# Kernel tuning notes

Hardware: AMD Instinct MI355X
Metric: run time of the kernel (lower is better)

The kernel has to match this reference:

```python
import jax, jax.numpy as jnp
import numpy as np

N, E, L, HID, HEADS, G = 50000, 800000, 2, 128, 8, 256
DK = HID // HEADS

def _ln(x, g, b, eps=1e-5):
    m = jnp.mean(x, axis=-1, keepdims=True)
    v = jnp.mean((x - m) ** 2, axis=-1, keepdims=True)
    return (x - m) * jax.lax.rsqrt(v + eps) * g + b

def setup_inputs() -> dict:
    key = jax.random.key(0)
    ks = jax.random.split(key, 24)
    rn = lambda i, s: (0.05 * jax.random.normal(ks[i], s)).astype(jnp.float32)
    return {
        'node_attr': jax.random.randint(ks[0], (N, 4), 0, 64, dtype=jnp.int32),
        'batch_idx': jnp.sort(jax.random.randint(ks[1], (N,), 0, G, dtype=jnp.int32)),
        'edge_index': jax.random.randint(ks[2], (2, E), 0, N, dtype=jnp.int32),
        'strat_dist': jax.random.randint(ks[3], (E,), 0, 32, dtype=jnp.int32),
        'strat_path': jax.random.randint(ks[4], (E,), 0, 16, dtype=jnp.int32),
        'atom_emb': rn(5, (4, 64, HID)),
        'dist_emb': rn(6, (L, 32, HID)),
        'path_emb': rn(7, (L, 16, HID)),
        'Wq': rn(8, (L, HID, HID)), 'bq': rn(9, (L, HID)),
        'Wk': rn(10, (L, HID, HID)), 'bk': rn(11, (L, HID)),
        'Wv': rn(12, (L, HID, HID)), 'bv': rn(13, (L, HID)),
        'Wa': rn(14, (L, HID, HID)), 'ba': rn(15, (L, HID)),
        'ln1_g': jnp.ones((L, HID), jnp.float32), 'ln1_b': jnp.zeros((L, HID), jnp.float32),
        'Wmid': rn(16, (L, HID, 2 * HID)), 'bmid': rn(17, (L, 2 * HID)),
        'Wo': rn(18, (L, 2 * HID, HID)), 'bo': rn(19, (L, HID)),
        'ln2_g': jnp.ones((L, HID), jnp.float32), 'ln2_b': jnp.zeros((L, HID), jnp.float32),
        'W_out': rn(20, (HID, 1)), 'b_out': jnp.zeros((1,), jnp.float32),
    }

def reference(node_attr, batch_idx, edge_index, strat_dist, strat_path,
              atom_emb, dist_emb, path_emb, Wq, bq, Wk, bk, Wv, bv, Wa, ba,
              ln1_g, ln1_b, Wmid, bmid, Wo, bo, ln2_g, ln2_b, W_out, b_out):
    # node encoder: sum of per-feature embeddings (AtomEncoder style)
    x = sum(atom_emb[f][node_attr[:, f]] for f in range(node_attr.shape[1]))  # [N, HID]
    src, tgt = edge_index[0], edge_index[1]  # j (source), i (target)
    inv_sqrt_dk = np.float32(1.0 / np.sqrt(DK))
    for l in range(L):
        # per-edge gather + relational encodings added to the source vector
        s = x[src] + dist_emb[l][strat_dist] + path_emb[l][strat_path]  # [E, HID]
        t = x[tgt]                                                      # [E, HID]
        q = (t @ Wq[l] + bq[l]).reshape(E, HEADS, DK)
        k = (s @ Wk[l] + bk[l]).reshape(E, HEADS, DK)
        v = (s @ Wv[l] + bv[l]).reshape(E, HEADS, DK)
        scores = jnp.sum(q * k, axis=-1) * inv_sqrt_dk  # [E, HEADS]
        # segment softmax keyed on target node id
        smax = jax.ops.segment_max(scores, tgt, num_segments=N)
        ex = jnp.exp(scores - smax[tgt])
        den = jax.ops.segment_sum(ex, tgt, num_segments=N)
        att = ex / (den[tgt] + 1e-16)                   # [E, HEADS]
        msg = (v * att[:, :, None]).reshape(E, HID)
        aggr = jax.ops.segment_sum(msg, tgt, num_segments=N)  # scatter-add
        # update: attn FFN + residual + LayerNorms (dropout is identity in eval)
        h = _ln(jax.nn.gelu(aggr, approximate=False) @ Wa[l] + ba[l] + x, ln1_g[l], ln1_b[l])
        h2 = jax.nn.gelu(h @ Wmid[l] + bmid[l], approximate=False) @ Wo[l] + bo[l]
        x = _ln(h2 + h, ln2_g[l], ln2_b[l])
    # global mean pool per graph, then readout
    cnt = jax.ops.segment_sum(jnp.ones((N,), x.dtype), batch_idx, num_segments=G)
    pooled = jax.ops.segment_sum(x, batch_idx, num_segments=G) / jnp.maximum(cnt, 1.0)[:, None]
    return pooled @ W_out + b_out
```

## Files before the change

kernel.cpp:

```cpp
#include <hip/hip_runtime.h>
#include <hip/hip_bf16.h>
#include <math.h>
#include <stdint.h>

#define N_NODES 50000
#define N_EDGES 800000
#define HID 128
#define NGRAPH 256
#define NLAYER 2
#define CAP 64

typedef __bf16 bf16x8 __attribute__((ext_vector_type(8)));
typedef __bf16 bf16x2 __attribute__((ext_vector_type(2)));
typedef float f32x4 __attribute__((ext_vector_type(4)));
typedef float f32x2 __attribute__((ext_vector_type(2)));

__device__ __forceinline__ float gelu_f(float v) {
    return 0.5f * v * (1.0f + erff(v * 0.70710678118654752f));
}

__device__ __forceinline__ void cvt4_fp8(uint32_t w, float* o) {
    f32x2 lo = __builtin_amdgcn_cvt_pk_f32_fp8(w, false);
    f32x2 hi = __builtin_amdgcn_cvt_pk_f32_fp8(w, true);
    o[0] = lo[0]; o[1] = lo[1]; o[2] = hi[0]; o[3] = hi[1];
}
__device__ __forceinline__ uint32_t pk4_fp8(float a, float b, float c, float d) {
    int w = __builtin_amdgcn_cvt_pk_fp8_f32(a, b, 0, false);
    w = __builtin_amdgcn_cvt_pk_fp8_f32(c, d, w, true);
    return (uint32_t)w;
}

__global__ __launch_bounds__(256) void prep_kernel(
    const int* __restrict__ attr, const float* __restrict__ aemb,
    __bf16* __restrict__ xb,
    const float* __restrict__ de, const float* __restrict__ pe,
    const float* __restrict__ Wk, const float* __restrict__ Wv,
    __bf16* __restrict__ tkv,
    const float* __restrict__ Wq, const float* __restrict__ Wa,
    const float* __restrict__ Wmid, const float* __restrict__ Wo,
    __bf16* __restrict__ wqkvf, __bf16* __restrict__ waf,
    __bf16* __restrict__ wmidf, __bf16* __restrict__ wof,
    const int* __restrict__ batch, const float* __restrict__ bout,
    const float* __restrict__ bq, const float* __restrict__ bk,
    const float* __restrict__ bv,
    float* __restrict__ invc, float* __restrict__ outp, float* __restrict__ bqkv) {
    __shared__ float sde[128];
    int b = blockIdx.x;
    int tid = threadIdx.x;
    if (b < 25000) {
        int idx = b * 256 + tid;
        int n = idx >> 7, c = idx & 127;
        const int4 a = *(const int4*)(attr + n * 4);
        float s = aemb[(0 * 64 + a.x) * 128 + c] + aemb[(1 * 64 + a.y) * 128 + c] +
                  aemb[(2 * 64 + a.z) * 128 + c] + aemb[(3 * 64 + a.w) * 128 + c];
        xb[idx] = (__bf16)s;
    } else if (b < 26024) {
        int bb = b - 25000;
        int l = bb >> 9;
        int md = bb & 511;
        int dd = md >> 4, pp = md & 15;
        int c = tid;
        if (c < 128) sde[c] = de[l * 4096 + dd * 128 + c] + pe[l * 2048 + pp * 128 + c];
        __syncthreads();
        const float* W = (c < 128) ? (Wk + l * 16384) : (Wv + l * 16384);
        int cc = c & 127;
        float acc = 0.f;
#pragma unroll 4
        for (int k = 0; k < 128; k++) acc = fmaf(sde[k], W[k * 128 + cc], acc);
        tkv[(size_t)bb * 256 + c] = (__bf16)acc;
    } else if (b < 26152) {
        int u = (b - 26024) * 256 + tid;
        int l = u >> 14, r = u & 16383;
        const float* srcp;
        __bf16* dstp;
        int kg, scol, srcCO;
        if (r < 6144) {
            kg = r / 384;
            int uu = r % 384;
            int sec = uu >> 7, cc = uu & 127;
            scol = ((cc & 15) << 3) | (cc >> 4);
            const float* Ws = (sec == 0) ? Wq : (sec == 1) ? Wk : Wv;
            srcp = Ws + l * 16384;
            srcCO = 128;
            dstp = wqkvf + (size_t)l * 49152 + (size_t)r * 8;
        } else if (r < 8192) {
            int rr = r - 6144;
            kg = rr >> 7;
            int cc = rr & 127;
            scol = ((cc & 15) << 3) | (cc >> 4);
            srcp = Wa + l * 16384;
            srcCO = 128;
            dstp = waf + (size_t)l * 16384 + (size_t)rr * 8;
        } else if (r < 12288) {
            int rr = r - 8192;
            kg = rr >> 8;
            int uu = rr & 255;
            int blk = uu >> 7, cc = uu & 127;
            scol = blk * 128 + (((cc & 15) << 3) | (cc >> 4));
            srcp = Wmid + l * 32768;
            srcCO = 256;
            dstp = wmidf + (size_t)l * 32768 + (size_t)rr * 8;
        } else {
            int rr = r - 12288;
            kg = rr >> 7;
            int cc = rr & 127;
            scol = ((cc & 15) << 3) | (cc >> 4);
            srcp = Wo + l * 32768;
            srcCO = 128;
            dstp = wof + (size_t)l * 32768 + (size_t)rr * 8;
        }
        bf16x8 o;
#pragma unroll
        for (int j = 0; j < 8; j++) o[j] = (__bf16)srcp[(kg * 8 + j) * srcCO + scol];
        *(bf16x8*)dstp = o;
    } else {
        int sb = b - 26152;
        if (sb == 0) {
            int g = tid;
            int lo = 0, hi = N_NODES;
            while (lo < hi) { int mid = (lo + hi) >> 1; if (batch[mid] < g) lo = mid + 1; else hi = mid; }
            int start = lo;
            lo = start; hi = N_NODES;
            while (lo < hi) { int mid = (lo + hi) >> 1; if (batch[mid] < g + 1) lo = mid + 1; else hi = mid; }
            int c2 = lo - start;
            invc[g] = 1.0f / fmaxf((float)c2, 1.0f);
            outp[g] = bout[0];
        } else {
            int r = (sb - 1) * 256 + tid;
            int l = r / 384, c = r % 384;
            float v = (c < 128) ? bq[l * 128 + c]
                    : (c < 256) ? bk[l * 128 + c - 128]
                                : bv[l * 128 + c - 256];
            bqkv[r] = v;
        }
    }
}

#define SCATB 1563
__global__ __launch_bounds__(256) void qkv_gemm(
    const __bf16* __restrict__ A, const __bf16* __restrict__ Wf,
    const float* __restrict__ bias, __bf16* __restrict__ Qb,
    uint8_t* __restrict__ kv8, int M, int scatN,
    const int* __restrict__ tgt, const int* __restrict__ src,
    const int* __restrict__ sd, const int* __restrict__ sp,
    int* __restrict__ cnt, uint32_t* __restrict__ ei) {
    int tid = threadIdx.x;
    if (blockIdx.x < (unsigned)scatN) {
        int e0 = blockIdx.x * 512 + tid;
        int e1 = e0 + 256;
        bool v1 = e1 < N_EDGES;
        bool v0 = e0 < N_EDGES;
        int t0 = 0, t1 = 0;
        uint32_t p0 = 0, p1 = 0;
        if (v0) {
            t0 = tgt[e0];
            p0 = (uint32_t)src[e0] | ((uint32_t)((sd[e0] << 4) | sp[e0]) << 16);
        }
        if (v1) {
            t1 = tgt[e1];
            p1 = (uint32_t)src[e1] | ((uint32_t)((sd[e1] << 4) | sp[e1]) << 16);
        }
        int r0 = CAP, r1 = CAP;
        if (v0) r0 = atomicAdd(&cnt[t0], 1);
        if (v1) r1 = atomicAdd(&cnt[t1], 1);
        if (v0 && r0 < CAP) ei[(t0 << 6) + r0] = p0;
        if (v1 && r1 < CAP) ei[(t1 << 6) + r1] = p1;
        return;
    }
    int bq = blockIdx.x - scatN;
    int sec = bq % 3;
    int rowblk = bq / 3;
    int lane = tid & 63;
    int wv = tid >> 6;
    int row0 = rowblk * 64 + wv * 16;
    int col0 = sec * 128;
    if (row0 >= M) return;
    int quad = lane >> 4, tq = lane & 15;
    f32x4 acc[8] = {};
#pragma unroll
    for (int k0 = 0; k0 < 128; k0 += 32) {
        int rr = row0 + tq;
        if (rr >= M) rr = M - 1;
        bf16x8 af = *(const bf16x8*)(A + (size_t)rr * 128 + k0 + quad * 8);
#pragma unroll
        for (int nt = 0; nt < 8; nt++) {
            bf16x8 bfr = *(const bf16x8*)(Wf + ((size_t)((k0 >> 3) + quad) * 384 + col0 + nt * 16 + tq) * 8);
            acc[nt] = __builtin_amdgcn_mfma_f32_16x16x32_bf16(af, bfr, acc[nt], 0, 0, 0);
        }
    }
    int cb = tq * 8;
    float bia[8];
#pragma unroll
    for (int t = 0; t < 8; t++) bia[t] = bias[col0 + cb + t];
#pragma unroll
    for (int v = 0; v < 4; v++) {
        int rr = row0 + quad * 4 + v;
        if (rr >= M) continue;
        float val[8];
#pragma unroll
        for (int t = 0; t < 8; t++) val[t] = acc[t][v] + bia[t];
        if (sec == 0) {
            bf16x8 ov;
#pragma unroll
            for (int t = 0; t < 8; t++) ov[t] = (__bf16)val[t];
            *(bf16x8*)(Qb + (size_t)rr * 128 + cb) = ov;
        } else {
            uint2 st;
            st.x = pk4_fp8(val[0], val[1], val[2], val[3]);
            st.y = pk4_fp8(val[4], val[5], val[6], val[7]);
            *(uint2*)(kv8 + (size_t)rr * 256 + (sec - 1) * 128 + cb) = st;
        }
    }
}

template <int CI, bool GOUT, bool LN, bool POOL>
__global__ __launch_bounds__(256) void mfma_gemm(
    const __bf16* __restrict__ A, const __bf16* __restrict__ Wf,
    const float* __restrict__ bias, const __bf16* __restrict__ res,
    const float* __restrict__ lng, const float* __restrict__ lnb,
    __bf16* outb,
    const int* __restrict__ batch, const float* __restrict__ invc,
    const float* __restrict__ WoutV, float* __restrict__ outp,
    int M, int CO) {
    __shared__ float ps[POOL ? NGRAPH : 1];
    int lane = threadIdx.x & 63;
    int wv = threadIdx.x >> 6;
    int row0 = blockIdx.y * 64 + wv * 16;
    int col0 = blockIdx.x * 128;
    bool active = row0 < M;
    if (POOL) {
        ps[threadIdx.x] = 0.f;
        __syncthreads();
    } else if (!active) {
        return;
    }
    int quad = lane >> 4, tq = lane & 15;
    if (active) {
        f32x4 acc[8] = {};
#pragma unroll
        for (int k0 = 0; k0 < CI; k0 += 32) {
            int rr = row0 + tq;
            if (rr >= M) rr = M - 1;
            bf16x8 af = *(const bf16x8*)(A + (size_t)rr * CI + k0 + quad * 8);
#pragma unroll
            for (int nt = 0; nt < 8; nt++) {
                bf16x8 bfr = *(const bf16x8*)(Wf + ((size_t)((k0 >> 3) + quad) * CO + col0 + nt * 16 + tq) * 8);
                acc[nt] = __builtin_amdgcn_mfma_f32_16x16x32_bf16(af, bfr, acc[nt], 0, 0, 0);
            }
        }
        int cb = col0 + tq * 8;
        float bia[8] = {};
        if (bias) {
#pragma unroll
            for (int t = 0; t < 8; t++) bia[t] = bias[cb + t];
        }
        float gv[8], bv2[8];
        if (LN) {
#pragma unroll
            for (int t = 0; t < 8; t++) { gv[t] = lng[cb + t]; bv2[t] = lnb[cb + t]; }
        }
        float wo8[8];
        if (POOL) {
#pragma unroll
            for (int t = 0; t < 8; t++) wo8[t] = WoutV[cb + t];
        }
#pragma unroll
        for (int v = 0; v < 4; v++) {
            int rr = row0 + quad * 4 + v;
            if (rr >= M) continue;
            float val[8];
#pragma unroll
            for (int nt = 0; nt < 8; nt++) val[nt] = acc[nt][v] + bia[nt];
            if (res) {
                bf16x8 rv = *(const bf16x8*)(res + (size_t)rr * 128 + tq * 8);
#pragma unroll
                for (int t = 0; t < 8; t++) val[t] += (float)rv[t];
            }
            if (GOUT) {
#pragma unroll
                for (int t = 0; t < 8; t++) val[t] = gelu_f(val[t]);
            }
            if (LN) {
                float s = 0.f, s2 = 0.f;
#pragma unroll
                for (int t = 0; t < 8; t++) { s += val[t]; s2 = fmaf(val[t], val[t], s2); }
#pragma unroll
                for (int o = 1; o < 16; o <<= 1) {
                    s += __shfl_xor(s, o);
                    s2 += __shfl_xor(s2, o);
                }
                float m = s * (1.0f / 128.0f);
                float var = s2 * (1.0f / 128.0f) - m * m;
                float rs = rsqrtf(var + 1e-5f);
#pragma unroll
                for (int t = 0; t < 8; t++) val[t] = (val[t] - m) * rs * gv[t] + bv2[t];
            }
            if (outb) {
                bf16x8 ov;
#pragma unroll
                for (int t = 0; t < 8; t++) ov[t] = (__bf16)val[t];
                *(bf16x8*)(outb + (size_t)rr * CO + cb) = ov;
            }
            if (POOL) {
                float dot = 0.f;
#pragma unroll
                for (int t = 0; t < 8; t++) dot = fmaf(val[t], wo8[t], dot);
#pragma unroll
                for (int o = 1; o < 16; o <<= 1) dot += __shfl_xor(dot, o);
                if (tq == 0) {
                    int g = batch[rr];
                    atomicAdd(&ps[g], dot * invc[g]);
                }
            }
        }
    }
    if (POOL) {
        __syncthreads();
        float pv = ps[threadIdx.x];
        if (pv != 0.f) atomicAdd(&outp[threadIdx.x], pv);
    }
}

__global__ __launch_bounds__(256) void attn_kernel(
    const __bf16* __restrict__ Qb, const uint8_t* __restrict__ kv8,
    const __bf16* __restrict__ tkv,
    const int* __restrict__ cnt, const uint32_t* __restrict__ ei,
    __bf16* __restrict__ outb) {
    __shared__ float red[4][1376];
    int wv = threadIdx.x >> 6;
    int i = blockIdx.x * 4 + wv;
    int lane = threadIdx.x & 63;
    int slot = lane >> 3, h = lane & 7;
    int ch0 = h * 16;
    const __bf16* qp = Qb + (size_t)i * 128 + ch0;
    bf16x8 q0 = *(const bf16x8*)qp;
    bf16x8 q1 = *(const bf16x8*)(qp + 8);
    float qf[16];
#pragma unroll
    for (int t = 0; t < 8; t++) { qf[t] = (float)q0[t]; qf[8 + t] = (float)q1[t]; }
    int deg = cnt[i];
    if (deg > CAP) deg = CAP;
    int p0 = i << 6;
    int p1 = p0 + deg;
    float l = 0.f;
    float a[16] = {};
    int p = p0 + slot;
    uint32_t w1 = 0, w2 = 0;
    if (p < p1) w1 = ei[p];
    if (p + 8 < p1) w2 = ei[p + 8];
    uint4 kw, vw;
    bf16x8 t0, t1, u0, u1;
    {
        int j = w1 & 0xffff, md = w1 >> 16;
        const uint8_t* kr = kv8 + (size_t)j * 256 + ch0;
        kw = *(const uint4*)kr;
        vw = *(const uint4*)(kr + 128);
        const __bf16* tr = tkv + md * 256 + ch0;
        t0 = *(const bf16x8*)tr;
        t1 = *(const bf16x8*)(tr + 8);
        u0 = *(const bf16x8*)(tr + 128);
        u1 = *(const bf16x8*)(tr + 136);
    }
    while (p < p1) {
        uint4 kwn, vwn;
        bf16x8 t0n, t1n, u0n, u1n;
        {
            int j = w2 & 0xffff, md = w2 >> 16;
            const uint8_t* kr = kv8 + (size_t)j * 256 + ch0;
            kwn = *(const uint4*)kr;
            vwn = *(const uint4*)(kr + 128);
            const __bf16* tr = tkv + md * 256 + ch0;
            t0n = *(const bf16x8*)tr;
            t1n = *(const bf16x8*)(tr + 8);
            u0n = *(const bf16x8*)(tr + 128);
            u1n = *(const bf16x8*)(tr + 136);
        }
        uint32_t w3 = w2;
        if (p + 16 < p1) w3 = ei[p + 16];
        float kf[16], vf[16];
        cvt4_fp8(kw.x, kf + 0); cvt4_fp8(kw.y, kf + 4);
        cvt4_fp8(kw.z, kf + 8); cvt4_fp8(kw.w, kf + 12);
        cvt4_fp8(vw.x, vf + 0); cvt4_fp8(vw.y, vf + 4);
        cvt4_fp8(vw.z, vf + 8); cvt4_fp8(vw.w, vf + 12);
        float s = 0.f;
#pragma unroll
        for (int t = 0; t < 8; t++) {
            s = fmaf(qf[t], kf[t] + (float)t0[t], s);
            s = fmaf(qf[8 + t], kf[8 + t] + (float)t1[t], s);
        }
        float pe = __expf(s * 0.25f);
        l += pe;
#pragma unroll
        for (int t = 0; t < 8; t++) {
            a[t] = fmaf(pe, vf[t] + (float)u0[t], a[t]);
            a[8 + t] = fmaf(pe, vf[8 + t] + (float)u1[t], a[8 + t]);
        }
        kw = kwn; vw = vwn; t0 = t0n; t1 = t1n; u0 = u0n; u1 = u1n;
        w2 = w3;
        p += 8;
    }
    float* rw = red[wv] + slot * 172 + 20 * h;
    *(float4*)(rw + 0) = make_float4(a[0], a[1], a[2], a[3]);
    *(float4*)(rw + 4) = make_float4(a[4], a[5], a[6], a[7]);
    *(float4*)(rw + 8) = make_float4(a[8], a[9], a[10], a[11]);
    *(float4*)(rw + 12) = make_float4(a[12], a[13], a[14], a[15]);
    red[wv][slot * 172 + 156 + h] = l;
    asm volatile("" ::: "memory");
    int pc = 2 * lane + 4 * (lane >> 3);
    int hh = lane >> 3;
    float s0 = 0.f, s1 = 0.f, ls = 0.f;
#pragma unroll
    for (int s = 0; s < 8; s++) {
        float2 v = *(const float2*)(red[wv] + s * 172 + pc);
        s0 += v.x;
        s1 += v.y;
        ls += red[wv][s * 172 + 156 + hh];
    }
    float inv = 1.0f / (ls + 1e-16f);
    bf16x2 o2;
    o2[0] = (__bf16)gelu_f(s0 * inv);
    o2[1] = (__bf16)gelu_f(s1 * inv);
    *(bf16x2*)(outb + (size_t)i * 128 + 2 * lane) = o2;
}

extern "C" void kernel_launch(void* const* d_in, const int* in_sizes, int n_in,
                              void* d_out, int out_size, void* d_ws, size_t ws_size,
                              hipStream_t stream) {
    const int N = N_NODES, E = N_EDGES;
    const int* node_attr = (const int*)d_in[0];
    const int* batch_idx = (const int*)d_in[1];
    const int* edge_index = (const int*)d_in[2];
    const int* strat_dist = (const int*)d_in[3];
    const int* strat_path = (const int*)d_in[4];
    const float* atom_emb = (const float*)d_in[5];
    const float* dist_emb = (const float*)d_in[6];
    const float* path_emb = (const float*)d_in[7];
    const float* Wq = (const float*)d_in[8];
    const float* bq = (const float*)d_in[9];
    const float* Wk = (const float*)d_in[10];
    const float* bk = (const float*)d_in[11];
    const float* Wv = (const float*)d_in[12];
    const float* bv = (const float*)d_in[13];
    const float* Wa = (const float*)d_in[14];
    const float* ba = (const float*)d_in[15];
    const float* ln1g = (const float*)d_in[16];
    const float* ln1b = (const float*)d_in[17];
    const float* Wmid = (const float*)d_in[18];
    const float* bmid = (const float*)d_in[19];
    const float* Wo = (const float*)d_in[20];
    const float* bo = (const float*)d_in[21];
    const float* ln2g = (const float*)d_in[22];
    const float* ln2b = (const float*)d_in[23];
    const float* Wout = (const float*)d_in[24];
    const float* bout = (const float*)d_in[25];
    float* out = (float*)d_out;

    const int* src = edge_index;
    const int* tgt = edge_index + E;

    size_t NF = (size_t)N * HID;
    float* invc = (float*)d_ws;
    float* bqkv = invc + 256;
    __bf16* xb = (__bf16*)(bqkv + 768);
    __bf16* Qb = xb + NF;
    __bf16* ab = Qb + NF;
    __bf16* midb = ab + NF;
    __bf16* tkv = midb + 2 * NF;
    __bf16* wqkvf = tkv + 262144;
    __bf16* waf = wqkvf + 98304;
    __bf16* wmidf = waf + 32768;
    __bf16* wof = wmidf + 65536;
    uint8_t* kv8 = (uint8_t*)(wof + 65536);
    uint32_t* ei = (uint32_t*)(kv8 + (size_t)N * 256);
    int* cnt = (int*)(ei + (size_t)N * CAP);

    hipMemsetAsync(cnt, 0, N * sizeof(int), stream);
    prep_kernel<<<26156, 256, 0, stream>>>(
        node_attr, atom_emb, xb,
        dist_emb, path_emb, Wk, Wv, tkv,
        Wq, Wa, Wmid, Wo, wqkvf, waf, wmidf, wof,
        batch_idx, bout, bq, bk, bv, invc, out, bqkv);

    const int GB = (N + 63) / 64;
    const int AB = (N + 3) / 4;

    for (int l = 0; l < NLAYER; ++l) {
        int scatN = (l == 0) ? SCATB : 0;
        qkv_gemm<<<scatN + 3 * GB, 256, 0, stream>>>(
            xb, wqkvf + l * 49152, bqkv + l * 384, Qb, kv8, N, scatN,
            tgt, src, strat_dist, strat_path, cnt, ei);

        attn_kernel<<<AB, 256, 0, stream>>>(Qb, kv8, tkv + l * 131072, cnt, ei, ab);

        mfma_gemm<128, false, true, false><<<dim3(1, GB), 256, 0, stream>>>(
            ab, waf + l * 16384, ba + l * 128, xb, ln1g + l * 128, ln1b + l * 128,
            ab, nullptr, nullptr, nullptr, nullptr, N, 128);
        mfma_gemm<128, true, false, false><<<dim3(2, GB), 256, 0, stream>>>(
            ab, wmidf + l * 32768, bmid + l * 256, nullptr, nullptr, nullptr,
            midb, nullptr, nullptr, nullptr, nullptr, N, 256);
        if (l < NLAYER - 1) {
            mfma_gemm<256, false, true, false><<<dim3(1, GB), 256, 0, stream>>>(
                midb, wof + l * 32768, bo + l * 128, ab, ln2g + l * 128, ln2b + l * 128,
                xb, nullptr, nullptr, nullptr, nullptr, N, 128);
        } else {
            mfma_gemm<256, false, true, true><<<dim3(1, GB), 256, 0, stream>>>(
                midb, wof + l * 32768, bo + l * 128, ab, ln2g + l * 128, ln2b + l * 128,
                nullptr, batch_idx, invc, Wout, out, N, 128);
        }
    }
}
```

Baseline: 429.4 us.

## Split QKV and Wmid GEMM columns across more blocks, pad degree counters

Halves the output columns per block in the QKV GEMM and in a new dedicated Wmid GEMM kernel, doubling the grid so more waves run concurrently with fewer accumulators each. The in-degree counters are also padded to a 16-int stride so that atomics on different targets do not contend on the same cache line. The costs are more redundant A-tile loads, narrower stores, and a larger counter memset.

After: 451.0 us. +5.0%, slower.

```diff
diff --git a/kernel.cpp b/kernel.cpp
--- a/kernel.cpp
+++ b/kernel.cpp
@@ -9,8 +9,10 @@
 #define NGRAPH 256
 #define NLAYER 2
 #define CAP 64
+#define CNTS 16
 
 typedef __bf16 bf16x8 __attribute__((ext_vector_type(8)));
+typedef __bf16 bf16x4 __attribute__((ext_vector_type(4)));
 typedef __bf16 bf16x2 __attribute__((ext_vector_type(2)));
 typedef float f32x4 __attribute__((ext_vector_type(4)));
 typedef float f32x2 __attribute__((ext_vector_type(2)));
@@ -148,8 +150,7 @@
     if (blockIdx.x < (unsigned)scatN) {
         int e0 = blockIdx.x * 512 + tid;
         int e1 = e0 + 256;
-        bool v1 = e1 < N_EDGES;
-        bool v0 = e0 < N_EDGES;
+        bool v0 = e0 < N_EDGES, v1 = e1 < N_EDGES;
         int t0 = 0, t1 = 0;
         uint32_t p0 = 0, p1 = 0;
         if (v0) {
@@ -161,54 +162,52 @@
             p1 = (uint32_t)src[e1] | ((uint32_t)((sd[e1] << 4) | sp[e1]) << 16);
         }
         int r0 = CAP, r1 = CAP;
-        if (v0) r0 = atomicAdd(&cnt[t0], 1);
-        if (v1) r1 = atomicAdd(&cnt[t1], 1);
+        if (v0) r0 = atomicAdd(&cnt[t0 * CNTS], 1);
+        if (v1) r1 = atomicAdd(&cnt[t1 * CNTS], 1);
         if (v0 && r0 < CAP) ei[(t0 << 6) + r0] = p0;
         if (v1 && r1 < CAP) ei[(t1 << 6) + r1] = p1;
         return;
     }
     int bq = blockIdx.x - scatN;
-    int sec = bq % 3;
-    int rowblk = bq / 3;
+    int sec = bq % 6;
+    int rowblk = bq / 6;
+    int S = sec >> 1, H = sec & 1;
     int lane = tid & 63;
     int wv = tid >> 6;
     int row0 = rowblk * 64 + wv * 16;
-    int col0 = sec * 128;
     if (row0 >= M) return;
     int quad = lane >> 4, tq = lane & 15;
-    f32x4 acc[8] = {};
+    f32x4 acc[4] = {};
 #pragma unroll
     for (int k0 = 0; k0 < 128; k0 += 32) {
         int rr = row0 + tq;
         if (rr >= M) rr = M - 1;
         bf16x8 af = *(const bf16x8*)(A + (size_t)rr * 128 + k0 + quad * 8);
 #pragma unroll
-        for (int nt = 0; nt < 8; nt++) {
-            bf16x8 bfr = *(const bf16x8*)(Wf + ((size_t)((k0 >> 3) + quad) * 384 + col0 + nt * 16 + tq) * 8);
+        for (int nt = 0; nt < 4; nt++) {
+            bf16x8 bfr = *(const bf16x8*)(Wf + ((size_t)((k0 >> 3) + quad) * 384 + S * 128 + H * 64 + nt * 16 + tq) * 8);
             acc[nt] = __builtin_amdgcn_mfma_f32_16x16x32_bf16(af, bfr, acc[nt], 0, 0, 0);
         }
     }
-    int cb = tq * 8;
-    float bia[8];
-#pragma unroll
-    for (int t = 0; t < 8; t++) bia[t] = bias[col0 + cb + t];
+    int cb = tq * 8 + H * 4;
+    float bia[4];
+#pragma unroll
+    for (int t = 0; t < 4; t++) bia[t] = bias[S * 128 + cb + t];
 #pragma unroll
     for (int v = 0; v < 4; v++) {
         int rr = row0 + quad * 4 + v;
         if (rr >= M) continue;
-        float val[8];
-#pragma unroll
-        for (int t = 0; t < 8; t++) val[t] = acc[t][v] + bia[t];
-        if (sec == 0) {
-            bf16x8 ov;
-#pragma unroll
-            for (int t = 0; t < 8; t++) ov[t] = (__bf16)val[t];
-            *(bf16x8*)(Qb + (size_t)rr * 128 + cb) = ov;
+        float val[4];
+#pragma unroll
+        for (int t = 0; t < 4; t++) val[t] = acc[t][v] + bia[t];
+        if (S == 0) {
+            bf16x4 ov;
+#pragma unroll
+            for (int t = 0; t < 4; t++) ov[t] = (__bf16)val[t];
+            *(bf16x4*)(Qb + (size_t)rr * 128 + cb) = ov;
         } else {
-            uint2 st;
-            st.x = pk4_fp8(val[0], val[1], val[2], val[3]);
-            st.y = pk4_fp8(val[4], val[5], val[6], val[7]);
-            *(uint2*)(kv8 + (size_t)rr * 256 + (sec - 1) * 128 + cb) = st;
+            *(uint32_t*)(kv8 + (size_t)rr * 256 + (S - 1) * 128 + cb) =
+                pk4_fp8(val[0], val[1], val[2], val[3]);
         }
     }
 }
@@ -321,6 +320,43 @@
     }
 }
 
+__global__ __launch_bounds__(256) void wmid_gemm(
+    const __bf16* __restrict__ A, const __bf16* __restrict__ Wf,
+    const float* __restrict__ bias, __bf16* __restrict__ outb, int M) {
+    int lane = threadIdx.x & 63;
+    int wv = threadIdx.x >> 6;
+    int row0 = blockIdx.y * 64 + wv * 16;
+    int c4 = blockIdx.x;
+    int S = c4 >> 1, H = c4 & 1;
+    if (row0 >= M) return;
+    int quad = lane >> 4, tq = lane & 15;
+    f32x4 acc[4] = {};
+#pragma unroll
+    for (int k0 = 0; k0 < 128; k0 += 32) {
+        int rr = row0 + tq;
+        if (rr >= M) rr = M - 1;
+        bf16x8 af = *(const bf16x8*)(A + (size_t)rr * 128 + k0 + quad * 8);
+#pragma unroll
+        for (int nt = 0; nt < 4; nt++) {
+            bf16x8 bfr = *(const bf16x8*)(Wf + ((size_t)((k0 >> 3) + quad) * 256 + S * 128 + H * 64 + nt * 16 + tq) * 8);
+            acc[nt] = __builtin_amdgcn_mfma_f32_16x16x32_bf16(af, bfr, acc[nt], 0, 0, 0);
+        }
+    }
+    int cb = S * 128 + tq * 8 + H * 4;
+    float bia[4];
+#pragma unroll
+    for (int t = 0; t < 4; t++) bia[t] = bias[cb + t];
+#pragma unroll
+    for (int v = 0; v < 4; v++) {
+        int rr = row0 + quad * 4 + v;
+        if (rr >= M) continue;
+        bf16x4 ov;
+#pragma unroll
+        for (int t = 0; t < 4; t++) ov[t] = (__bf16)gelu_f(acc[t][v] + bia[t]);
+        *(bf16x4*)(outb + (size_t)rr * 256 + cb) = ov;
+    }
+}
+
 __global__ __launch_bounds__(256) void attn_kernel(
     const __bf16* __restrict__ Qb, const uint8_t* __restrict__ kv8,
     const __bf16* __restrict__ tkv,
@@ -338,7 +374,7 @@
     float qf[16];
 #pragma unroll
     for (int t = 0; t < 8; t++) { qf[t] = (float)q0[t]; qf[8 + t] = (float)q1[t]; }
-    int deg = cnt[i];
+    int deg = cnt[i * CNTS];
     if (deg > CAP) deg = CAP;
     int p0 = i << 6;
     int p1 = p0 + deg;
@@ -474,7 +510,7 @@
     uint32_t* ei = (uint32_t*)(kv8 + (size_t)N * 256);
     int* cnt = (int*)(ei + (size_t)N * CAP);
 
-    hipMemsetAsync(cnt, 0, N * sizeof(int), stream);
+    hipMemsetAsync(cnt, 0, (size_t)N * CNTS * sizeof(int), stream);
     prep_kernel<<<26156, 256, 0, stream>>>(
         node_attr, atom_emb, xb,
         dist_emb, path_emb, Wk, Wv, tkv,
@@ -486,7 +522,7 @@
 
     for (int l = 0; l < NLAYER; ++l) {
         int scatN = (l == 0) ? SCATB : 0;
-        qkv_gemm<<<scatN + 3 * GB, 256, 0, stream>>>(
+        qkv_gemm<<<scatN + 6 * GB, 256, 0, stream>>>(
             xb, wqkvf + l * 49152, bqkv + l * 384, Qb, kv8, N, scatN,
             tgt, src, strat_dist, strat_path, cnt, ei);
 
@@ -495,9 +531,8 @@
         mfma_gemm<128, false, true, false><<<dim3(1, GB), 256, 0, stream>>>(
             ab, waf + l * 16384, ba + l * 128, xb, ln1g + l * 128, ln1b + l * 128,
             ab, nullptr, nullptr, nullptr, nullptr, N, 128);
-        mfma_gemm<128, true, false, false><<<dim3(2, GB), 256, 0, stream>>>(
-            ab, wmidf + l * 32768, bmid + l * 256, nullptr, nullptr, nullptr,
-            midb, nullptr, nullptr, nullptr, nullptr, N, 256);
+        wmid_gemm<<<dim3(4, GB), 256, 0, stream>>>(
+            ab, wmidf + l * 32768, bmid + l * 256, midb, N);
         if (l < NLAYER - 1) {
             mfma_gemm<256, false, true, false><<<dim3(1, GB), 256, 0, stream>>>(
                 midb, wof + l * 32768, bo + l * 128, ab, ln2g + l * 128, ln2b + l * 128,
```
